# Kernel optimization log

Hardware: AMD Instinct MI355X
Metric: run time of the kernel (lower is better)

Reference implementation:

```python
import jax, jax.numpy as jnp
import numpy as np

N, D, IN, HID, OUT, E = 20000, 8, 64, 128, 64, 100000
EPS = 1e-5


def _bn(h, g, b):
    # training-mode BatchNorm1d: biased batch variance, eps=1e-5
    m = h.mean(axis=0)
    v = jnp.mean((h - m) ** 2, axis=0)
    return (h - m) * jax.lax.rsqrt(v + EPS) * g + b


def setup_inputs() -> dict:
    key = jax.random.key(0)
    ks = jax.random.split(key, 12)
    x = jax.random.normal(ks[0], (N, IN), dtype=jnp.float32)
    node_ts = jax.random.uniform(ks[1], (N,), dtype=jnp.float32)
    neighbor_idx = jax.random.randint(ks[2], (N, D), 0, N, dtype=jnp.int32)
    neighbor_ts = jax.random.uniform(ks[3], (N, D), dtype=jnp.float32)
    target = jax.random.randint(ks[4], (2, E), 0, N, dtype=jnp.int32)
    neg_pairs = jax.random.randint(ks[5], (2, E), 0, N, dtype=jnp.int32)
    W1 = jax.random.normal(ks[6], (IN, HID), dtype=jnp.float32) * (1.0 / np.sqrt(IN))
    b1 = jnp.zeros((HID,), jnp.float32)
    g1 = jnp.ones((HID,), jnp.float32)
    be1 = jnp.zeros((HID,), jnp.float32)
    W2 = jax.random.normal(ks[7], (HID, OUT), dtype=jnp.float32) * (1.0 / np.sqrt(HID))
    b2 = jnp.zeros((OUT,), jnp.float32)
    g2 = jnp.ones((OUT,), jnp.float32)
    be2 = jnp.zeros((OUT,), jnp.float32)
    Wd = jax.random.normal(ks[8], (OUT, 1), dtype=jnp.float32) * (1.0 / np.sqrt(OUT))
    bd = jnp.zeros((1,), jnp.float32)
    return {"x": x, "node_ts": node_ts, "neighbor_idx": neighbor_idx,
            "neighbor_ts": neighbor_ts, "target": target, "neg_pairs": neg_pairs,
            "W1": W1, "b1": b1, "g1": g1, "be1": be1,
            "W2": W2, "b2": b2, "g2": g2, "be2": be2, "Wd": Wd, "bd": bd}


def reference(x, node_ts, neighbor_idx, neighbor_ts, target, neg_pairs,
              W1, b1, g1, be1, W2, b2, g2, be2, Wd, bd):
    n = jnp.arange(N, dtype=neighbor_idx.dtype)
    # ---- level-2 queries: every node at its own timestamp ----
    # children = D temporal-neighbor slots + self (self always valid, ts=node_ts)
    c_idx = jnp.concatenate([neighbor_idx, n[:, None]], axis=1)          # [N, D+1]
    c_ts = jnp.concatenate([neighbor_ts, node_ts[:, None]], axis=1)      # [N, D+1]
    mask2 = jnp.concatenate([neighbor_ts <= node_ts[:, None],
                             jnp.ones((N, 1), bool)], axis=1)            # [N, D+1]
    # ---- level-1 queries: each (child node, child ts) pair ----
    ci = c_idx.reshape(-1)                                               # [M]
    cts = c_ts.reshape(-1)
    gc_idx = jnp.concatenate([neighbor_idx[ci], ci[:, None]], axis=1)    # [M, D+1]
    mask1 = jnp.concatenate([neighbor_ts[ci] <= cts[:, None],
                             jnp.ones((ci.shape[0], 1), bool)], axis=1)
    # ---- layer 0: raw features of grandchildren ----
    h0 = x[gc_idx]                                                       # [M, D+1, IN]
    m1 = mask1.astype(x.dtype)
    agg1 = jnp.einsum('mk,mkf->mf', m1, h0) / m1.sum(1, keepdims=True)   # masked mean
    h1 = jax.nn.relu(_bn(agg1 @ W1 + b1, g1, be1))                       # [M, HID]
    h1 = h1.reshape(N, D + 1, HID)
    # ---- layer 2 aggregation over temporal children ----
    m2 = mask2.astype(x.dtype)
    agg2 = jnp.einsum('nk,nkf->nf', m2, h1) / m2.sum(1, keepdims=True)
    embs = jax.nn.relu(_bn(agg2 @ W2 + b2, g2, be2))                     # [N, OUT]
    # ---- HadNet link decoder + BCEWithLogits ----
    pos = (embs[target[0]] * embs[target[1]]) @ Wd + bd                  # [E, 1]
    neg = (embs[neg_pairs[0]] * embs[neg_pairs[1]]) @ Wd + bd            # [E, 1]
    preds = jnp.concatenate([pos, neg], axis=0)[:, 0]                    # [2E]
    labels = jnp.concatenate([jnp.ones((E,), x.dtype), jnp.zeros((E,), x.dtype)])
    loss = jnp.mean(jnp.maximum(preds, 0.0) - preds * labels
                    + jnp.log1p(jnp.exp(-jnp.abs(preds))))
    return loss
```

## Files before the change

### kernel.cpp

```cpp
#include <hip/hip_runtime.h>
#include <math.h>

constexpr int kN = 20000;
constexpr int kD = 8;
constexpr int kE = 100000;
constexpr int kM = kN * 9;
constexpr int kTiles1 = kM / 16;
constexpr int kTiles3 = kN / 16;
constexpr float kEps = 1e-5f;

constexpr int S_SUM1 = 0, S_SQ1 = 128, S_SUM2 = 256, S_SQ2 = 320;
constexpr int P_SC1 = 384, P_SH1 = 512, P_SC2 = 640, P_SH2 = 704;

constexpr size_t OFF_AGG2  = 46080000;
constexpr size_t OFF_PRE2  = 51200000;
constexpr size_t OFF_EMBS  = 56320000;
constexpr size_t OFF_STATS = 61440000;

typedef short short8 __attribute__((ext_vector_type(8)));
typedef float floatx4 __attribute__((ext_vector_type(4)));

__device__ __forceinline__ unsigned f2bf(float f) {
  unsigned u = __float_as_uint(f);
  u += 0x7fffu + ((u >> 16) & 1u);
  return u >> 16;
}

__global__ __launch_bounds__(256, 3) void k1_gather_gemm1(
    const float* __restrict__ x, const float* __restrict__ node_ts,
    const int* __restrict__ nidx, const float* __restrict__ nts,
    const float* __restrict__ W1, const float* __restrict__ b1,
    unsigned short* __restrict__ pre1,
    float* __restrict__ stats)
{
  __shared__ unsigned short W1T[128 * 64];
  __shared__ unsigned short atile[4][16 * 64];
  __shared__ float redS[256][8];
  __shared__ float redQ[256][8];

  const int tid = threadIdx.x;
  const int lane = tid & 63;
  const int wave = tid >> 6;
  const int l15 = lane & 15;
  const int q = lane >> 4;

  for (int i = tid; i < 8192; i += 256) {
    int n = i >> 6, k = i & 63;
    W1T[i] = (unsigned short)f2bf(W1[k * 128 + n]);
  }
  __syncthreads();

  short8 bf[8][2];
#pragma unroll
  for (int c = 0; c < 8; ++c)
#pragma unroll
    for (int s = 0; s < 2; ++s)
      bf[c][s] = *(const short8*)&W1T[(c * 16 + l15) * 64 + q * 8 + s * 32];

  float b1c[8];
#pragma unroll
  for (int c = 0; c < 8; ++c) b1c[c] = b1[c * 16 + l15];

  float sum8[8], sq8[8];
#pragma unroll
  for (int c = 0; c < 8; ++c) { sum8[c] = 0.f; sq8[c] = 0.f; }

  const int gw = blockIdx.x * 4 + wave;
  const int nw = gridDim.x * 4;

  for (int t = gw; t < kTiles1; t += nw) {
    const int r0 = t * 16;
#pragma unroll 2
    for (int r = 0; r < 16; ++r) {
      int m = r0 + r;
      int n = (int)((unsigned)m / 9u);
      int slot = m - n * 9;
      int c; float tt;
      if (slot < kD) { c = nidx[n * kD + slot]; tt = nts[n * kD + slot]; }
      else           { c = n;                   tt = node_ts[n]; }
      float s = x[c * 64 + lane];
      float fcnt = 1.f;
#pragma unroll
      for (int j = 0; j < kD; ++j) {
        float w = (nts[c * kD + j] <= tt) ? 1.f : 0.f;
        s = fmaf(w, x[nidx[c * kD + j] * 64 + lane], s);
        fcnt += w;
      }
      atile[wave][r * 64 + lane] = (unsigned short)f2bf(s / fcnt);
    }
    short8 af0 = *(const short8*)&atile[wave][l15 * 64 + q * 8];
    short8 af1 = *(const short8*)&atile[wave][l15 * 64 + q * 8 + 32];

    floatx4 acc[8];
#pragma unroll
    for (int c = 0; c < 8; ++c) {
      acc[c] = (floatx4){0.f, 0.f, 0.f, 0.f};
      acc[c] = __builtin_amdgcn_mfma_f32_16x16x32_bf16(af0, bf[c][0], acc[c], 0, 0, 0);
      acc[c] = __builtin_amdgcn_mfma_f32_16x16x32_bf16(af1, bf[c][1], acc[c], 0, 0, 0);
    }
#pragma unroll
    for (int c = 0; c < 8; ++c) {
      int col = c * 16 + l15;
#pragma unroll
      for (int i = 0; i < 4; ++i) {
        float v = acc[c][i] + b1c[c];
        int row = r0 + q * 4 + i;
        pre1[row * 128 + col] = (unsigned short)f2bf(v);
        sum8[c] += v; sq8[c] += v * v;
      }
    }
  }

  __syncthreads();
#pragma unroll
  for (int c = 0; c < 8; ++c) { redS[tid][c] = sum8[c]; redQ[tid][c] = sq8[c]; }
  __syncthreads();
  if (tid < 128) {
    int c = tid >> 4, r15 = tid & 15;
    float s = 0.f, qq = 0.f;
#pragma unroll
    for (int w = 0; w < 4; ++w)
#pragma unroll
      for (int p = 0; p < 4; ++p) {
        int T = w * 64 + p * 16 + r15;
        s += redS[T][c]; qq += redQ[T][c];
      }
    atomicAdd(&stats[S_SUM1 + tid], s);
    atomicAdd(&stats[S_SQ1 + tid], qq);
  }
}

__global__ void k2_fin1(float* stats, const float* __restrict__ g1,
                        const float* __restrict__ be1) {
  int c = threadIdx.x;
  float mean = stats[S_SUM1 + c] * (1.f / kM);
  float var  = stats[S_SQ1 + c] * (1.f / kM) - mean * mean;
  float sc   = g1[c] * rsqrtf(var + kEps);
  stats[P_SC1 + c] = sc;
  stats[P_SH1 + c] = be1[c] - mean * sc;
}

__global__ __launch_bounds__(256) void k3a_agg2(
    const unsigned* __restrict__ pre1dw, const float* __restrict__ node_ts,
    const float* __restrict__ nts, const float* __restrict__ stats,
    unsigned* __restrict__ agg2dw)
{
  const int n = blockIdx.x * 4 + (threadIdx.x >> 6);
  const int L = threadIdx.x & 63;
  const float sc0 = stats[P_SC1 + 2 * L], sc1 = stats[P_SC1 + 2 * L + 1];
  const float sh0 = stats[P_SH1 + 2 * L], sh1 = stats[P_SH1 + 2 * L + 1];
  const float tn = node_ts[n];
  float s0 = 0.f, s1 = 0.f, fcnt = 0.f;
#pragma unroll
  for (int slot = 0; slot < 9; ++slot) {
    float w = (slot < kD) ? ((nts[n * kD + slot] <= tn) ? 1.f : 0.f) : 1.f;
    unsigned u = pre1dw[(n * 9 + slot) * 64 + L];
    float p0 = __uint_as_float(u << 16);
    float p1 = __uint_as_float(u & 0xffff0000u);
    s0 += w * fmaxf(fmaf(p0, sc0, sh0), 0.f);
    s1 += w * fmaxf(fmaf(p1, sc1, sh1), 0.f);
    fcnt += w;
  }
  float r = 1.f / fcnt;
  agg2dw[n * 64 + L] = f2bf(s0 * r) | (f2bf(s1 * r) << 16);
}

__global__ __launch_bounds__(256, 3) void k3b_gemm2(
    const unsigned short* __restrict__ agg2, const float* __restrict__ W2,
    const float* __restrict__ b2, float* __restrict__ stats,
    float* __restrict__ pre2)
{
  __shared__ unsigned short W2T[64 * 128];
  __shared__ float redS[256][4];
  __shared__ float redQ[256][4];

  const int tid = threadIdx.x;
  const int lane = tid & 63;
  const int wave = tid >> 6;
  const int l15 = lane & 15;
  const int q = lane >> 4;

  for (int i = tid; i < 8192; i += 256) {
    int n = i >> 7, k = i & 127;
    W2T[i] = (unsigned short)f2bf(W2[k * 64 + n]);
  }
  __syncthreads();

  short8 bfr[4][4];
#pragma unroll
  for (int c = 0; c < 4; ++c)
#pragma unroll
    for (int s = 0; s < 4; ++s)
      bfr[c][s] = *(const short8*)&W2T[(c * 16 + l15) * 128 + q * 8 + s * 32];

  float b2c[4];
#pragma unroll
  for (int c = 0; c < 4; ++c) b2c[c] = b2[c * 16 + l15];

  float sum4[4], sq4[4];
#pragma unroll
  for (int c = 0; c < 4; ++c) { sum4[c] = 0.f; sq4[c] = 0.f; }

  const int gw = blockIdx.x * 4 + wave;
  const int nw = gridDim.x * 4;

  for (int t = gw; t < kTiles3; t += nw) {
    const int r0 = t * 16;
    short8 af[4];
#pragma unroll
    for (int s = 0; s < 4; ++s)
      af[s] = *(const short8*)&agg2[(r0 + l15) * 128 + q * 8 + s * 32];

    floatx4 acc[4];
#pragma unroll
    for (int c = 0; c < 4; ++c) {
      acc[c] = (floatx4){0.f, 0.f, 0.f, 0.f};
#pragma unroll
      for (int s = 0; s < 4; ++s)
        acc[c] = __builtin_amdgcn_mfma_f32_16x16x32_bf16(af[s], bfr[c][s], acc[c], 0, 0, 0);
    }
#pragma unroll
    for (int c = 0; c < 4; ++c) {
      int col = c * 16 + l15;
#pragma unroll
      for (int i = 0; i < 4; ++i) {
        float v = acc[c][i] + b2c[c];
        int row = r0 + q * 4 + i;
        pre2[row * 64 + col] = v;
        sum4[c] += v; sq4[c] += v * v;
      }
    }
  }

  __syncthreads();
#pragma unroll
  for (int c = 0; c < 4; ++c) { redS[tid][c] = sum4[c]; redQ[tid][c] = sq4[c]; }
  __syncthreads();
  if (tid < 64) {
    int c = tid >> 4, r15 = tid & 15;
    float s = 0.f, qq = 0.f;
#pragma unroll
    for (int w = 0; w < 4; ++w)
#pragma unroll
      for (int p = 0; p < 4; ++p) {
        int T = w * 64 + p * 16 + r15;
        s += redS[T][c]; qq += redQ[T][c];
      }
    atomicAdd(&stats[S_SUM2 + tid], s);
    atomicAdd(&stats[S_SQ2 + tid], qq);
  }
}

__global__ void k4_fin2(float* stats, const float* __restrict__ g2,
                        const float* __restrict__ be2) {
  int c = threadIdx.x;
  float mean = stats[S_SUM2 + c] * (1.f / kN);
  float var  = stats[S_SQ2 + c] * (1.f / kN) - mean * mean;
  float sc   = g2[c] * rsqrtf(var + kEps);
  stats[P_SC2 + c] = sc;
  stats[P_SH2 + c] = be2[c] - mean * sc;
}

__global__ __launch_bounds__(256) void k5_embs(
    const float* __restrict__ pre2, const float* __restrict__ stats,
    float* __restrict__ embs)
{
  int idx = blockIdx.x * 256 + threadIdx.x;
  int col = idx & 63;
  embs[idx] = fmaxf(fmaf(pre2[idx], stats[P_SC2 + col], stats[P_SH2 + col]), 0.f);
}

__global__ __launch_bounds__(256) void k6_loss(
    const float* __restrict__ embs, const int* __restrict__ tgt,
    const int* __restrict__ neg, const float* __restrict__ Wd,
    const float* __restrict__ bd, float* __restrict__ out)
{
  __shared__ float wds[64];
  __shared__ float redl[256];
  int tid = threadIdx.x;
  if (tid < 64) wds[tid] = Wd[tid];
  __syncthreads();
  int e = blockIdx.x * 256 + tid;
  float l = 0.f;
  if (e < 2 * kE) {
    int i, j; float lab;
    if (e < kE) { i = tgt[e];      j = tgt[kE + e]; lab = 1.f; }
    else        { i = neg[e - kE]; j = neg[e];      lab = 0.f; }
    const float4* a  = (const float4*)(embs + (size_t)i * 64);
    const float4* bb = (const float4*)(embs + (size_t)j * 64);
    const float4* wv = (const float4*)wds;
    float p = bd[0];
#pragma unroll
    for (int t = 0; t < 16; ++t) {
      float4 av = a[t], bv = bb[t], w4 = wv[t];
      p += (av.x * bv.x) * w4.x + (av.y * bv.y) * w4.y
         + (av.z * bv.z) * w4.z + (av.w * bv.w) * w4.w;
    }
    l = fmaxf(p, 0.f) - p * lab + log1pf(expf(-fabsf(p)));
  }
  redl[tid] = l;
  __syncthreads();
  for (int s = 128; s > 0; s >>= 1) {
    if (tid < s) redl[tid] += redl[tid + s];
    __syncthreads();
  }
  if (tid == 0) atomicAdd(out, redl[0] * (1.f / (2 * kE)));
}

extern "C" void kernel_launch(void* const* d_in, const int* in_sizes, int n_in,
                              void* d_out, int out_size, void* d_ws, size_t ws_size,
                              hipStream_t stream) {
  (void)in_sizes; (void)n_in; (void)out_size; (void)ws_size;
  const float* x       = (const float*)d_in[0];
  const float* node_ts = (const float*)d_in[1];
  const int*   nidx    = (const int*)d_in[2];
  const float* nts     = (const float*)d_in[3];
  const int*   tgt     = (const int*)d_in[4];
  const int*   neg     = (const int*)d_in[5];
  const float* W1      = (const float*)d_in[6];
  const float* b1      = (const float*)d_in[7];
  const float* g1      = (const float*)d_in[8];
  const float* be1     = (const float*)d_in[9];
  const float* W2      = (const float*)d_in[10];
  const float* b2      = (const float*)d_in[11];
  const float* g2      = (const float*)d_in[12];
  const float* be2     = (const float*)d_in[13];
  const float* Wd      = (const float*)d_in[14];
  const float* bd      = (const float*)d_in[15];

  char* ws = (char*)d_ws;
  unsigned short* pre1 = (unsigned short*)ws;
  unsigned short* agg2 = (unsigned short*)(ws + OFF_AGG2);
  float* pre2  = (float*)(ws + OFF_PRE2);
  float* embs  = (float*)(ws + OFF_EMBS);
  float* stats = (float*)(ws + OFF_STATS);
  float* out   = (float*)d_out;

  hipMemsetAsync(stats, 0, 384 * sizeof(float), stream);
  hipMemsetAsync(out, 0, sizeof(float), stream);

  k1_gather_gemm1<<<1408, 256, 0, stream>>>(x, node_ts, nidx, nts, W1, b1, pre1, stats);
  k2_fin1<<<1, 128, 0, stream>>>(stats, g1, be1);
  k3a_agg2<<<kN / 4, 256, 0, stream>>>((const unsigned*)pre1, node_ts, nts, stats,
                                       (unsigned*)agg2);
  k3b_gemm2<<<160, 256, 0, stream>>>(agg2, W2, b2, stats, pre2);
  k4_fin2<<<1, 64, 0, stream>>>(stats, g2, be2);
  k5_embs<<<kN * 64 / 256, 256, 0, stream>>>(pre2, stats, embs);
  k6_loss<<<(2 * kE + 255) / 256, 256, 0, stream>>>(embs, tgt, neg, Wd, bd, out);
}
```

Measured before the change: 249.2 us.

## Split gather from GEMM1, fold BN finalize kernels, pre-scale embeddings, cooperative loss

```diff
diff --git a/kernel.cpp b/kernel.cpp
--- a/kernel.cpp
+++ b/kernel.cpp
@@ -10,12 +10,13 @@
 constexpr float kEps = 1e-5f;
 
 constexpr int S_SUM1 = 0, S_SQ1 = 128, S_SUM2 = 256, S_SQ2 = 320;
-constexpr int P_SC1 = 384, P_SH1 = 512, P_SC2 = 640, P_SH2 = 704;
-
+
+constexpr size_t REG_B     = 23040000;
 constexpr size_t OFF_AGG2  = 46080000;
-constexpr size_t OFF_PRE2  = 51200000;
-constexpr size_t OFF_EMBS  = 56320000;
-constexpr size_t OFF_STATS = 61440000;
+constexpr size_t OFF_STATS = 51200000;
+constexpr size_t OFF_PRE2  = 0;
+constexpr size_t OFF_EMBS  = 5120000;
+constexpr size_t OFF_EMBSW = 10240000;
 
 typedef short short8 __attribute__((ext_vector_type(8)));
 typedef float floatx4 __attribute__((ext_vector_type(4)));
@@ -26,15 +27,41 @@
   return u >> 16;
 }
 
-__global__ __launch_bounds__(256, 3) void k1_gather_gemm1(
+__global__ __launch_bounds__(256) void k1a_gather(
     const float* __restrict__ x, const float* __restrict__ node_ts,
     const int* __restrict__ nidx, const float* __restrict__ nts,
+    unsigned short* __restrict__ agg1)
+{
+  const int m = blockIdx.x * 4 + (threadIdx.x >> 6);
+  const int lane = threadIdx.x & 63;
+  const int n = (int)((unsigned)m / 9u);
+  const int slot = m - n * 9;
+  int c; float t;
+  if (slot < kD) { c = nidx[n * kD + slot]; t = nts[n * kD + slot]; }
+  else           { c = n;                   t = node_ts[n]; }
+  c = __builtin_amdgcn_readfirstlane(c);
+  float s = x[c * 64 + lane];
+  float fcnt = 1.f;
+#pragma unroll
+  for (int j = 0; j < kD; ++j) {
+    int cj = nidx[c * kD + j];
+    float w = (nts[c * kD + j] <= t) ? 1.f : 0.f;
+    s = fmaf(w, x[cj * 64 + lane], s);
+    fcnt += w;
+  }
+  float v = s / fcnt;
+  const int tt = m >> 4, r = m & 15, g = lane >> 3, jj = lane & 7;
+  agg1[tt * 1024 + g * 128 + r * 8 + jj] = (unsigned short)f2bf(v);
+}
+
+__global__ __launch_bounds__(256, 3) void k1b_gemm1(
+    const unsigned short* aggA,
+    unsigned short* preLo,
+    unsigned short* __restrict__ preHi,
     const float* __restrict__ W1, const float* __restrict__ b1,
-    unsigned short* __restrict__ pre1,
     float* __restrict__ stats)
 {
-  __shared__ unsigned short W1T[128 * 64];
-  __shared__ unsigned short atile[4][16 * 64];
+  __shared__ unsigned short W1T[128 * 72];
   __shared__ float redS[256][8];
   __shared__ float redQ[256][8];
 
@@ -46,7 +73,7 @@
 
   for (int i = tid; i < 8192; i += 256) {
     int n = i >> 6, k = i & 63;
-    W1T[i] = (unsigned short)f2bf(W1[k * 128 + n]);
+    W1T[n * 72 + k] = (unsigned short)f2bf(W1[k * 128 + n]);
   }
   __syncthreads();
 
@@ -55,7 +82,7 @@
   for (int c = 0; c < 8; ++c)
 #pragma unroll
     for (int s = 0; s < 2; ++s)
-      bf[c][s] = *(const short8*)&W1T[(c * 16 + l15) * 64 + q * 8 + s * 32];
+      bf[c][s] = *(const short8*)&W1T[(c * 16 + l15) * 72 + q * 8 + s * 32];
 
   float b1c[8];
 #pragma unroll
@@ -69,27 +96,9 @@
   const int nw = gridDim.x * 4;
 
   for (int t = gw; t < kTiles1; t += nw) {
-    const int r0 = t * 16;
-#pragma unroll 2
-    for (int r = 0; r < 16; ++r) {
-      int m = r0 + r;
-      int n = (int)((unsigned)m / 9u);
-      int slot = m - n * 9;
-      int c; float tt;
-      if (slot < kD) { c = nidx[n * kD + slot]; tt = nts[n * kD + slot]; }
-      else           { c = n;                   tt = node_ts[n]; }
-      float s = x[c * 64 + lane];
-      float fcnt = 1.f;
-#pragma unroll
-      for (int j = 0; j < kD; ++j) {
-        float w = (nts[c * kD + j] <= tt) ? 1.f : 0.f;
-        s = fmaf(w, x[nidx[c * kD + j] * 64 + lane], s);
-        fcnt += w;
-      }
-      atile[wave][r * 64 + lane] = (unsigned short)f2bf(s / fcnt);
-    }
-    short8 af0 = *(const short8*)&atile[wave][l15 * 64 + q * 8];
-    short8 af1 = *(const short8*)&atile[wave][l15 * 64 + q * 8 + 32];
+    const unsigned short* ap = aggA + (size_t)t * 1024;
+    short8 af0 = *(const short8*)(ap + (q)*128 + l15 * 8);
+    short8 af1 = *(const short8*)(ap + (4 + q) * 128 + l15 * 8);
 
     floatx4 acc[8];
 #pragma unroll
@@ -100,12 +109,14 @@
     }
 #pragma unroll
     for (int c = 0; c < 8; ++c) {
-      int col = c * 16 + l15;
+      int colq = (c & 3) * 16 + l15;
 #pragma unroll
       for (int i = 0; i < 4; ++i) {
         float v = acc[c][i] + b1c[c];
-        int row = r0 + q * 4 + i;
-        pre1[row * 128 + col] = (unsigned short)f2bf(v);
+        int row = t * 16 + q * 4 + i;
+        unsigned short hv = (unsigned short)f2bf(v);
+        if (c < 4) preLo[(size_t)row * 64 + colq] = hv;
+        else       preHi[(size_t)row * 64 + colq] = hv;
         sum8[c] += v; sq8[c] += v * v;
       }
     }
@@ -130,31 +141,33 @@
   }
 }
 
-__global__ void k2_fin1(float* stats, const float* __restrict__ g1,
-                        const float* __restrict__ be1) {
-  int c = threadIdx.x;
-  float mean = stats[S_SUM1 + c] * (1.f / kM);
-  float var  = stats[S_SQ1 + c] * (1.f / kM) - mean * mean;
-  float sc   = g1[c] * rsqrtf(var + kEps);
-  stats[P_SC1 + c] = sc;
-  stats[P_SH1 + c] = be1[c] - mean * sc;
-}
-
 __global__ __launch_bounds__(256) void k3a_agg2(
-    const unsigned* __restrict__ pre1dw, const float* __restrict__ node_ts,
-    const float* __restrict__ nts, const float* __restrict__ stats,
-    unsigned* __restrict__ agg2dw)
-{
-  const int n = blockIdx.x * 4 + (threadIdx.x >> 6);
-  const int L = threadIdx.x & 63;
-  const float sc0 = stats[P_SC1 + 2 * L], sc1 = stats[P_SC1 + 2 * L + 1];
-  const float sh0 = stats[P_SH1 + 2 * L], sh1 = stats[P_SH1 + 2 * L + 1];
+    const unsigned* __restrict__ loDW, const unsigned* __restrict__ hiDW,
+    const float* __restrict__ node_ts, const float* __restrict__ nts,
+    const float* __restrict__ stats, const float* __restrict__ g1,
+    const float* __restrict__ be1, unsigned* __restrict__ agg2dw)
+{
+  __shared__ float sc[128], sh[128];
+  const int tid = threadIdx.x;
+  if (tid < 128) {
+    float mean = stats[S_SUM1 + tid] * (1.f / kM);
+    float var  = stats[S_SQ1 + tid] * (1.f / kM) - mean * mean;
+    float s    = g1[tid] * rsqrtf(var + kEps);
+    sc[tid] = s; sh[tid] = be1[tid] - mean * s;
+  }
+  __syncthreads();
+  const int n = blockIdx.x * 4 + (tid >> 6);
+  const int L = tid & 63;
+  const unsigned* base = (L < 32) ? loDW : hiDW;
+  const int Lc = L & 31;
+  const float sc0 = sc[2 * L], sc1 = sc[2 * L + 1];
+  const float sh0 = sh[2 * L], sh1 = sh[2 * L + 1];
   const float tn = node_ts[n];
   float s0 = 0.f, s1 = 0.f, fcnt = 0.f;
 #pragma unroll
   for (int slot = 0; slot < 9; ++slot) {
     float w = (slot < kD) ? ((nts[n * kD + slot] <= tn) ? 1.f : 0.f) : 1.f;
-    unsigned u = pre1dw[(n * 9 + slot) * 64 + L];
+    unsigned u = base[(size_t)(n * 9 + slot) * 32 + Lc];
     float p0 = __uint_as_float(u << 16);
     float p1 = __uint_as_float(u & 0xffff0000u);
     s0 += w * fmaxf(fmaf(p0, sc0, sh0), 0.f);
@@ -170,7 +183,7 @@
     const float* __restrict__ b2, float* __restrict__ stats,
     float* __restrict__ pre2)
 {
-  __shared__ unsigned short W2T[64 * 128];
+  __shared__ unsigned short W2T[64 * 136];
   __shared__ float redS[256][4];
   __shared__ float redQ[256][4];
 
@@ -182,7 +195,7 @@
 
   for (int i = tid; i < 8192; i += 256) {
     int n = i >> 7, k = i & 127;
-    W2T[i] = (unsigned short)f2bf(W2[k * 64 + n]);
+    W2T[n * 136 + k] = (unsigned short)f2bf(W2[k * 64 + n]);
   }
   __syncthreads();
 
@@ -191,7 +204,7 @@
   for (int c = 0; c < 4; ++c)
 #pragma unroll
     for (int s = 0; s < 4; ++s)
-      bfr[c][s] = *(const short8*)&W2T[(c * 16 + l15) * 128 + q * 8 + s * 32];
+      bfr[c][s] = *(const short8*)&W2T[(c * 16 + l15) * 136 + q * 8 + s * 32];
 
   float b2c[4];
 #pragma unroll
@@ -209,7 +222,7 @@
     short8 af[4];
 #pragma unroll
     for (int s = 0; s < 4; ++s)
-      af[s] = *(const short8*)&agg2[(r0 + l15) * 128 + q * 8 + s * 32];
+      af[s] = *(const short8*)&agg2[(size_t)(r0 + l15) * 128 + q * 8 + s * 32];
 
     floatx4 acc[4];
 #pragma unroll
@@ -226,7 +239,7 @@
       for (int i = 0; i < 4; ++i) {
         float v = acc[c][i] + b2c[c];
         int row = r0 + q * 4 + i;
-        pre2[row * 64 + col] = v;
+        pre2[(size_t)row * 64 + col] = v;
         sum4[c] += v; sq4[c] += v * v;
       }
     }
@@ -251,54 +264,58 @@
   }
 }
 
-__global__ void k4_fin2(float* stats, const float* __restrict__ g2,
-                        const float* __restrict__ be2) {
-  int c = threadIdx.x;
-  float mean = stats[S_SUM2 + c] * (1.f / kN);
-  float var  = stats[S_SQ2 + c] * (1.f / kN) - mean * mean;
-  float sc   = g2[c] * rsqrtf(var + kEps);
-  stats[P_SC2 + c] = sc;
-  stats[P_SH2 + c] = be2[c] - mean * sc;
-}
-
 __global__ __launch_bounds__(256) void k5_embs(
     const float* __restrict__ pre2, const float* __restrict__ stats,
-    float* __restrict__ embs)
-{
-  int idx = blockIdx.x * 256 + threadIdx.x;
+    const float* __restrict__ g2, const float* __restrict__ be2,
+    const float* __restrict__ Wd, float* __restrict__ embs,
+    float* __restrict__ embsW)
+{
+  __shared__ float sc[64], sh[64], wd[64];
+  const int tid = threadIdx.x;
+  if (tid < 64) {
+    float mean = stats[S_SUM2 + tid] * (1.f / kN);
+    float var  = stats[S_SQ2 + tid] * (1.f / kN) - mean * mean;
+    float s    = g2[tid] * rsqrtf(var + kEps);
+    sc[tid] = s; sh[tid] = be2[tid] - mean * s; wd[tid] = Wd[tid];
+  }
+  __syncthreads();
+  int idx = blockIdx.x * 256 + tid;
   int col = idx & 63;
-  embs[idx] = fmaxf(fmaf(pre2[idx], stats[P_SC2 + col], stats[P_SH2 + col]), 0.f);
+  float e = fmaxf(fmaf(pre2[idx], sc[col], sh[col]), 0.f);
+  embs[idx] = e;
+  embsW[idx] = e * wd[col];
 }
 
 __global__ __launch_bounds__(256) void k6_loss(
-    const float* __restrict__ embs, const int* __restrict__ tgt,
-    const int* __restrict__ neg, const float* __restrict__ Wd,
+    const float* __restrict__ embs, const float* __restrict__ embsW,
+    const int* __restrict__ tgt, const int* __restrict__ neg,
     const float* __restrict__ bd, float* __restrict__ out)
 {
-  __shared__ float wds[64];
   __shared__ float redl[256];
-  int tid = threadIdx.x;
-  if (tid < 64) wds[tid] = Wd[tid];
-  __syncthreads();
-  int e = blockIdx.x * 256 + tid;
-  float l = 0.f;
-  if (e < 2 * kE) {
-    int i, j; float lab;
-    if (e < kE) { i = tgt[e];      j = tgt[kE + e]; lab = 1.f; }
-    else        { i = neg[e - kE]; j = neg[e];      lab = 0.f; }
-    const float4* a  = (const float4*)(embs + (size_t)i * 64);
-    const float4* bb = (const float4*)(embs + (size_t)j * 64);
-    const float4* wv = (const float4*)wds;
-    float p = bd[0];
-#pragma unroll
-    for (int t = 0; t < 16; ++t) {
-      float4 av = a[t], bv = bb[t], w4 = wv[t];
-      p += (av.x * bv.x) * w4.x + (av.y * bv.y) * w4.y
-         + (av.z * bv.z) * w4.z + (av.w * bv.w) * w4.w;
-    }
-    l = fmaxf(p, 0.f) - p * lab + log1pf(expf(-fabsf(p)));
-  }
-  redl[tid] = l;
+  const int tid = threadIdx.x;
+  const int tq = tid & 15;
+  const int qb = tid >> 4;
+  const float bd0 = bd[0];
+  float lsum = 0.f;
+  const int e0 = blockIdx.x * 128 + qb * 8;
+#pragma unroll
+  for (int it = 0; it < 8; ++it) {
+    int e = e0 + it;
+    if (e < 2 * kE) {
+      int i, j; float lab;
+      if (e < kE) { i = tgt[e];      j = tgt[kE + e]; lab = 1.f; }
+      else        { i = neg[e - kE]; j = neg[e];      lab = 0.f; }
+      float4 av = *(const float4*)(embsW + (size_t)i * 64 + tq * 4);
+      float4 bv = *(const float4*)(embs  + (size_t)j * 64 + tq * 4);
+      float p = av.x * bv.x + av.y * bv.y + av.z * bv.z + av.w * bv.w;
+      p += __shfl_xor(p, 1); p += __shfl_xor(p, 2);
+      p += __shfl_xor(p, 4); p += __shfl_xor(p, 8);
+      p += bd0;
+      float l = fmaxf(p, 0.f) - p * lab + log1pf(expf(-fabsf(p)));
+      if (tq == 0) lsum += l;
+    }
+  }
+  redl[tid] = lsum;
   __syncthreads();
   for (int s = 128; s > 0; s >>= 1) {
     if (tid < s) redl[tid] += redl[tid + s];
@@ -329,22 +346,23 @@
   const float* bd      = (const float*)d_in[15];
 
   char* ws = (char*)d_ws;
-  unsigned short* pre1 = (unsigned short*)ws;
-  unsigned short* agg2 = (unsigned short*)(ws + OFF_AGG2);
+  unsigned short* regA  = (unsigned short*)ws;
+  unsigned short* regB  = (unsigned short*)(ws + REG_B);
+  unsigned short* agg2  = (unsigned short*)(ws + OFF_AGG2);
+  float* stats = (float*)(ws + OFF_STATS);
   float* pre2  = (float*)(ws + OFF_PRE2);
   float* embs  = (float*)(ws + OFF_EMBS);
-  float* stats = (float*)(ws + OFF_STATS);
+  float* embsW = (float*)(ws + OFF_EMBSW);
   float* out   = (float*)d_out;
 
   hipMemsetAsync(stats, 0, 384 * sizeof(float), stream);
   hipMemsetAsync(out, 0, sizeof(float), stream);
 
-  k1_gather_gemm1<<<1408, 256, 0, stream>>>(x, node_ts, nidx, nts, W1, b1, pre1, stats);
-  k2_fin1<<<1, 128, 0, stream>>>(stats, g1, be1);
-  k3a_agg2<<<kN / 4, 256, 0, stream>>>((const unsigned*)pre1, node_ts, nts, stats,
-                                       (unsigned*)agg2);
+  k1a_gather<<<kM / 4, 256, 0, stream>>>(x, node_ts, nidx, nts, regA);
+  k1b_gemm1<<<704, 256, 0, stream>>>(regA, regA, regB, W1, b1, stats);
+  k3a_agg2<<<kN / 4, 256, 0, stream>>>((const unsigned*)regA, (const unsigned*)regB,
+                                       node_ts, nts, stats, g1, be1, (unsigned*)agg2);
   k3b_gemm2<<<160, 256, 0, stream>>>(agg2, W2, b2, stats, pre2);
-  k4_fin2<<<1, 64, 0, stream>>>(stats, g2, be2);
-  k5_embs<<<kN * 64 / 256, 256, 0, stream>>>(pre2, stats, embs);
-  k6_loss<<<(2 * kE + 255) / 256, 256, 0, stream>>>(embs, tgt, neg, Wd, bd, out);
-}
+  k5_embs<<<kN * 64 / 256, 256, 0, stream>>>(pre2, stats, g2, be2, Wd, embs, embsW);
+  k6_loss<<<(2 * kE + 127) / 128, 256, 0, stream>>>(embs, embsW, tgt, neg, bd, out);
+}
```

Result: faster. 220.8 us (-11.4%).
